# Performance work log

Measured on AMD Instinct MI355X. Metric: run time of the kernel, lower is better.

Reference implementation:

```python
import jax, jax.numpy as jnp
import numpy as np
import math

HEADS = 8
HID = 32
MODES = 8
IN_CH = 4
SEQ = 32
B = 2
H = 64
W = 64


def spectral_conv(x, wr, wi):
    # x: [N, Cin, H, W]; w: [Cin, Cout, m, m] complex (low rfft2 modes only)
    n, _, h, w = x.shape
    m = wr.shape[2]
    xf = jnp.fft.rfft2(x)  # [N, Cin, H, W//2+1] complex64
    of = jnp.einsum('bixy,ioxy->boxy', xf[:, :, :m, :m], wr + 1j * wi)
    out_ft = jnp.zeros((n, wr.shape[1], h, w // 2 + 1), dtype=of.dtype)
    out_ft = out_ft.at[:, :, :m, :m].set(of)
    return jnp.fft.irfft2(out_ft, s=(h, w))


def conv1x1(x, w, b):
    # x: [N, Cin, H, W], w: [Cout, Cin], b: [Cout]
    return jnp.einsum('bchw,oc->bohw', x, w) + b[None, :, None, None]


def setup_inputs() -> dict:
    key = jax.random.key(0)
    ks = jax.random.split(key, 16)
    hd = HEADS * HID
    s = 0.02
    inp = {
        'v': jax.random.normal(ks[0], (B, SEQ, IN_CH, H, W), dtype=jnp.float32),
        'qwr': jax.random.normal(ks[1], (IN_CH, hd, MODES, MODES), dtype=jnp.float32) * s,
        'qwi': jax.random.normal(ks[2], (IN_CH, hd, MODES, MODES), dtype=jnp.float32) * s,
        'kwr': jax.random.normal(ks[3], (IN_CH, hd, MODES, MODES), dtype=jnp.float32) * s,
        'kwi': jax.random.normal(ks[4], (IN_CH, hd, MODES, MODES), dtype=jnp.float32) * s,
        'vwr': jax.random.normal(ks[5], (IN_CH, hd, MODES, MODES), dtype=jnp.float32) * s,
        'vwi': jax.random.normal(ks[6], (IN_CH, hd, MODES, MODES), dtype=jnp.float32) * s,
        'u1wr': jax.random.normal(ks[7], (hd, HID, MODES, MODES), dtype=jnp.float32) * s,
        'u1wi': jax.random.normal(ks[8], (hd, HID, MODES, MODES), dtype=jnp.float32) * s,
        'u2wr': jax.random.normal(ks[9], (HID, IN_CH, MODES, MODES), dtype=jnp.float32) * s,
        'u2wi': jax.random.normal(ks[10], (HID, IN_CH, MODES, MODES), dtype=jnp.float32) * s,
        's1w': jax.random.normal(ks[11], (HID, hd), dtype=jnp.float32) * s,
        's1b': jnp.zeros((HID,), dtype=jnp.float32),
        's2w': jax.random.normal(ks[12], (IN_CH, HID), dtype=jnp.float32) * s,
        's2b': jnp.zeros((IN_CH,), dtype=jnp.float32),
    }
    return inp


def reference(v, qwr, qwi, kwr, kwi, vwr, vwi, u1wr, u1wi, u2wr, u2wi, s1w, s1b, s2w, s2b):
    b, s, c, h, w = v.shape
    scale = 1.0 / math.sqrt(HID / HEADS)
    vr = v.reshape(b * s, c, h, w)
    embed = (b, HEADS, s, -1, h, w)  # same raw row-major reshape as torch
    q = spectral_conv(vr, qwr, qwi).reshape(embed)
    k = spectral_conv(vr, kwr, kwi).reshape(embed)
    val = spectral_conv(vr, vwr, vwi).reshape(embed)
    # inner products over channel dim, then dx^2-weighted spatial integral
    ip = jnp.einsum('bhsdrc,bhtdrc->bhstrc', q, k) * scale
    dx = 1.0 / h
    l2 = jnp.sum(ip, axis=(-2, -1)) * (dx * dx)  # [b, h, s1, s2]
    A = jax.nn.softmax(l2, axis=-1)
    u = jnp.einsum('bhst,bhtdrc->bhsdrc', A, val)
    u = jnp.transpose(u, (0, 2, 1, 3, 4, 5)).reshape(b * s, HEADS * u.shape[3], h, w)
    # SimpleFNO: gelu(conv1) + skip1, then conv2 + skip2
    x1 = jax.nn.gelu(spectral_conv(u, u1wr, u1wi), approximate=False) + conv1x1(u, s1w, s1b)
    x2 = spectral_conv(x1, u2wr, u2wi) + conv1x1(x1, s2w, s2b)
    return x2.reshape(b, s, c, h, w)
```

## Files before the change

### kernel.cpp

```cpp
#include <hip/hip_runtime.h>
#include <math.h>

#define HEADS 8
#define HIDC  32
#define MODES 8
#define IN_CH 4
#define SEQ   32
#define NS    64
#define HD    256
#define NM    64
#define NPIX  4096
#define TWO_PI_D 6.283185307179586476925286766559

__device__ __forceinline__ float2 f2(float a, float b){ return make_float2(a,b); }

__global__ __launch_bounds__(256) void fwd_dft_kernel(const float* __restrict__ src,
                                                      float2* __restrict__ dst){
  int f = blockIdx.x;
  const float* fld = src + (size_t)f * NPIX;
  __shared__ float  s_fld[64*65];
  __shared__ float2 s_cs[64];
  __shared__ float2 s_a1[64][8];
  int tid = threadIdx.x;
  for (int k = tid; k < NPIX; k += 256) s_fld[(k>>6)*65 + (k&63)] = fld[k];
  if (tid < 64){ double sv, cv; sincos(TWO_PI_D * tid / 64.0, &sv, &cv); s_cs[tid] = f2((float)cv,(float)sv); }
  __syncthreads();
  for (int o = tid; o < 512; o += 256){
    int y = o >> 3, kx = o & 7;
    const float* row = s_fld + y*65;
    float sr = 0.f, si = 0.f;
    for (int x = 0; x < 64; ++x){
      float2 cs = s_cs[(kx*x) & 63];
      float v = row[x];
      sr += v * cs.x; si -= v * cs.y;
    }
    s_a1[y][kx] = f2(sr, si);
  }
  __syncthreads();
  if (tid < 64){
    int ky = tid >> 3, kx = tid & 7;
    float sr = 0.f, si = 0.f;
    for (int y = 0; y < 64; ++y){
      float2 a = s_a1[y][kx];
      float2 cs = s_cs[(ky*y) & 63];
      sr += a.x*cs.x + a.y*cs.y;
      si += a.y*cs.x - a.x*cs.y;
    }
    dst[(size_t)f*NM + tid] = f2(sr, si);
  }
}

__global__ __launch_bounds__(256) void gram_kernel(const float* __restrict__ qwr, const float* __restrict__ qwi,
                                                   const float* __restrict__ kwr, const float* __restrict__ kwi,
                                                   float2* __restrict__ G2, float* __restrict__ Gdc){
  int m = blockIdx.x, tid = threadIdx.x;
  __shared__ float qsr[4][257], qsi[4][257], ksr[4][257], ksi[4][257];
  for (int k = tid; k < 1024; k += 256){
    int i = k >> 8, c = k & 255;
    size_t a = ((size_t)(i*256 + c))*64 + m;
    qsr[i][c] = qwr[a]; qsi[i][c] = qwi[a];
    ksr[i][c] = kwr[a]; ksi[i][c] = kwi[a];
  }
  __syncthreads();
  int kx = m & 7, ky = m >> 3;
  float w = (kx >= 1) ? 2.0f : ((ky >= 1) ? 0.5f : 0.0f);
  for (int e = tid; e < 1024; e += 256){
    int P = e >> 7, T = (e >> 4) & 7, i = (e >> 2) & 3, j = e & 3;
    float grr=0.f, gri=0.f, gir=0.f, gii=0.f;
    for (int d = 0; d < 32; ++d){
      float ar = qsr[i][P*32+d], ai = qsi[i][P*32+d];
      float br = ksr[j][T*32+d], bi = ksi[j][T*32+d];
      grr += ar*br; gri += ar*bi; gir += ai*br; gii += ai*bi;
    }
    G2[(size_t)(((m*8+P)*4+i)*4+j)*8 + T] = f2(w*(grr+gii), w*(gir-gri));
    if (m == 0){
      int o = ((P*4+i)*4+j)*8 + T;
      Gdc[o] = grr; Gdc[1024+o] = gri; Gdc[2048+o] = gir; Gdc[3072+o] = gii;
    }
  }
}

__global__ __launch_bounds__(256) void attn_kernel(const float2* __restrict__ Vf,
                                                   const float2* __restrict__ G2,
                                                   const float* __restrict__ Gdc,
                                                   float* __restrict__ A){
  int bx = blockIdx.x;
  int s = bx & 31;
  int base = ((bx >> 8) * 32) + (((bx >> 5) & 7) * 4);
  int tid = threadIdx.x;
  int t = tid & 31, mc = tid >> 5;
  __shared__ float2 s_vf[4][IN_CH][64];
  __shared__ float  s_part[8][33];
  for (int k = tid; k < 4*IN_CH*64; k += 256){
    int m = k & 63, c = (k>>6)&3, smp = k>>8;
    s_vf[smp][c][m] = Vf[((size_t)(base+smp)*IN_CH + c)*NM + m];
  }
  __syncthreads();
  int sg = s >> 3, P = s & 7;
  int tg = t >> 3, T = t & 7;
  float acc = 0.f;
  for (int mm = 0; mm < 8; ++mm){
    int m = mc*8 + mm;
    const float2* g = G2 + (size_t)((m*8+P)*16)*8 + T;
    float sub = 0.f;
    for (int i = 0; i < 4; ++i){
      float2 a = s_vf[sg][i][m];
      for (int j = 0; j < 4; ++j){
        float2 b = s_vf[tg][j][m];
        float zr = a.x*b.x + a.y*b.y;
        float zi = a.y*b.x - a.x*b.y;
        float2 gv = g[(size_t)(i*4+j)*8];
        sub += zr*gv.x - zi*gv.y;
      }
    }
    acc += sub;
  }
  if (mc == 0){
    float sub = 0.f;
    for (int i = 0; i < 4; ++i){
      float2 a = s_vf[sg][i][0];
      for (int j = 0; j < 4; ++j){
        float2 b = s_vf[tg][j][0];
        int o = ((P*4+i)*4+j)*8 + T;
        sub += a.x*b.x*Gdc[o] - a.x*b.y*Gdc[1024+o]
             - a.y*b.x*Gdc[2048+o] + a.y*b.y*Gdc[3072+o];
      }
    }
    acc += sub;
  }
  s_part[mc][t] = acc;
  __syncthreads();
  if (tid < 32){
    float l2 = 0.f;
    for (int k = 0; k < 8; ++k) l2 += s_part[k][tid];
    l2 *= 0.5f / (4096.0f * 4096.0f);
    float mx = l2;
    for (int off = 16; off; off >>= 1) mx = fmaxf(mx, __shfl_xor(mx, off, 32));
    float e = expf(l2 - mx);
    float sm = e;
    for (int off = 16; off; off >>= 1) sm += __shfl_xor(sm, off, 32);
    A[(size_t)bx*32 + tid] = e / sm;
  }
}

__global__ __launch_bounds__(256) void uspec_kernel(const float2* __restrict__ Vf,
                                                    const float* __restrict__ vwr, const float* __restrict__ vwi,
                                                    const float* __restrict__ A,
                                                    float2* __restrict__ Uf){
  int bid = blockIdx.x;
  int mg = bid & 31, hh = (bid >> 5) & 7, b = bid >> 8;
  int m0 = mg*2;
  int nbase = b*32 + hh*4;
  int tid = threadIdx.x;
  __shared__ float2 s_vw[4][2][256];
  __shared__ float2 s_vv[4][2][256];
  __shared__ float  s_A[32][33];
  __shared__ float2 s_vf[4][4][2];
  for (int k = tid; k < 2048; k += 256){
    int i = k >> 9, mm = (k >> 8) & 1, c = k & 255;
    size_t a = ((size_t)i*256 + c)*64 + m0 + mm;
    s_vw[i][mm][c] = f2(vwr[a], vwi[a]);
  }
  for (int k = tid; k < 1024; k += 256)
    s_A[k>>5][k&31] = A[(size_t)((b*8+hh)*32 + (k>>5))*32 + (k&31)];
  if (tid < 32){
    int smp = tid >> 3, i = (tid >> 1) & 3, mm = tid & 1;
    s_vf[smp][i][mm] = Vf[((size_t)(nbase+smp)*4 + i)*64 + m0 + mm];
  }
  __syncthreads();
  for (int k = tid; k < 2048; k += 256){
    int smp = k >> 9, mm = (k >> 8) & 1, c = k & 255;
    float sr = 0.f, si = 0.f;
    for (int i = 0; i < 4; ++i){
      float2 v = s_vf[smp][i][mm];
      float2 w = s_vw[i][mm][c];
      sr += v.x*w.x - v.y*w.y;
      si += v.x*w.y + v.y*w.x;
    }
    s_vv[smp][mm][c] = f2(sr, si);
  }
  __syncthreads();
  int sg = tid >> 5, d = tid & 31;
  float2 acc[4][2];
  for (int ss = 0; ss < 4; ++ss)
    for (int mm = 0; mm < 2; ++mm) acc[ss][mm] = f2(0.f, 0.f);
  for (int tt = 0; tt < 32; ++tt){
    int tg = tt >> 3, c = (tt & 7)*32 + d;
    float a0 = s_A[sg*4+0][tt], a1 = s_A[sg*4+1][tt];
    float a2 = s_A[sg*4+2][tt], a3 = s_A[sg*4+3][tt];
    for (int mm = 0; mm < 2; ++mm){
      float2 v = s_vv[tg][mm][c];
      acc[0][mm].x += a0*v.x; acc[0][mm].y += a0*v.y;
      acc[1][mm].x += a1*v.x; acc[1][mm].y += a1*v.y;
      acc[2][mm].x += a2*v.x; acc[2][mm].y += a2*v.y;
      acc[3][mm].x += a3*v.x; acc[3][mm].y += a3*v.y;
    }
  }
  for (int ss = 0; ss < 4; ++ss){
    int n = b*32 + sg*4 + ss;
    for (int mm = 0; mm < 2; ++mm)
      Uf[((size_t)n*64 + m0 + mm)*256 + hh*32 + d] = acc[ss][mm];
  }
}

__global__ __launch_bounds__(256) void u1t_kernel(const float* __restrict__ u1wr,
                                                  const float* __restrict__ u1wi,
                                                  float4* __restrict__ u1wT){
  int t = blockIdx.x*256 + threadIdx.x;
  int o1 = t & 31, c = (t>>5) & 255, m = t >> 13;
  float pr = ((m & 7)==0 && m) ? 0.5f : 1.0f;
  float pi = m ? pr : 0.0f;
  size_t src = ((size_t)c*32 + o1)*64 + m;
  float wr = u1wr[src], wi = u1wi[src];
  u1wT[t] = make_float4(pr*wr, pi*wi, pr*wi, pi*wr);
}

__global__ __launch_bounds__(128) void mix1_kernel(const float2* __restrict__ Uf,
                                                   const float4* __restrict__ u1wT,
                                                   const float* __restrict__ s1w,
                                                   float2* __restrict__ U1f, float2* __restrict__ S1f){
  int n = blockIdx.x >> 4, mg = blockIdx.x & 15, m0 = mg*4;
  int tid = threadIdx.x;
  __shared__ float2 s_u[4][256];
  for (int k = tid; k < 1024; k += 128){
    int mm = k >> 8, c = k & 255;
    s_u[mm][c] = Uf[((size_t)n*64 + m0 + mm)*256 + c];
  }
  __syncthreads();
  int o1 = tid & 31, mm = tid >> 5;
  int m = m0 + mm;
  const float4* wp = u1wT + (size_t)m*256*32 + o1;
  const float* swp = s1w + o1*256;
  float2 au = f2(0.f,0.f), asv = f2(0.f,0.f);
  #pragma unroll 8
  for (int c = 0; c < 256; ++c){
    float2 u = s_u[mm][c];
    float4 w = wp[(size_t)c*32];
    float sw = swp[c];
    au.x  += u.x*w.x - u.y*w.y;
    au.y  += u.x*w.z + u.y*w.w;
    asv.x += u.x*sw;
    asv.y += u.y*sw;
  }
  size_t ob = ((size_t)n*32 + o1)*64 + m;
  U1f[ob] = au; S1f[ob] = asv;
}

__global__ __launch_bounds__(256) void x1dft_kernel(const float2* __restrict__ U1f,
                                                    const float2* __restrict__ S1f,
                                                    const float* __restrict__ s1b,
                                                    float* __restrict__ x1,
                                                    float2* __restrict__ X1f){
  int f = blockIdx.x, o1 = f & 31, tid = threadIdx.x;
  __shared__ float2 s_e[64][8];
  __shared__ float2 s_gu[64], s_gs[64];
  __shared__ float2 s_tu[64][8], s_ts[64][8];
  __shared__ float  s_fld[64*68];
  __shared__ float2 s_a1[64][8];
  for (int e = tid; e < 512; e += 256){
    int a = e >> 3, b = e & 7;
    double sv, cv; sincos(TWO_PI_D * ((a*b) & 63) / 64.0, &sv, &cv);
    s_e[a][b] = f2((float)cv, (float)sv);
  }
  if (tid >= 128 && tid < 192) s_gu[tid-128] = U1f[(size_t)f*NM + tid-128];
  else if (tid >= 192) s_gs[tid-192] = S1f[(size_t)f*NM + tid-192];
  __syncthreads();
  for (int o = tid; o < 512; o += 256){
    int y = o >> 3, kx = o & 7;
    float wf = (kx ? 2.0f : 1.0f) * (1.0f/4096.0f);
    float ar=0.f, ai=0.f, br=0.f, bi=0.f;
    for (int ky = 0; ky < 8; ++ky){
      float2 cs = s_e[y][ky];
      float2 gu = s_gu[ky*8+kx], gs = s_gs[ky*8+kx];
      ar += gu.x*cs.x - gu.y*cs.y;  ai += gu.x*cs.y + gu.y*cs.x;
      br += gs.x*cs.x - gs.y*cs.y;  bi += gs.x*cs.y + gs.y*cs.x;
    }
    s_tu[y][kx] = f2(ar*wf, ai*wf);
    s_ts[y][kx] = f2(br*wf, bi*wf);
  }
  __syncthreads();
  int xx = tid & 63;
  float2 ce[8];
  {
    const float4* ep = (const float4*)&s_e[xx][0];
    float4 e0 = ep[0], e1 = ep[1], e2 = ep[2], e3 = ep[3];
    ce[0]=f2(e0.x,e0.y); ce[1]=f2(e0.z,e0.w);
    ce[2]=f2(e1.x,e1.y); ce[3]=f2(e1.z,e1.w);
    ce[4]=f2(e2.x,e2.y); ce[5]=f2(e2.z,e2.w);
    ce[6]=f2(e3.x,e3.y); ce[7]=f2(e3.z,e3.w);
  }
  float bias = s1b[o1];
  float* dst = x1 + (size_t)f*NPIX;
  for (int i = 0; i < 16; ++i){
    int p = i*256 + tid;
    int y = p >> 6;
    const float4* tp = (const float4*)&s_tu[y][0];
    float4 t0 = tp[0], t1 = tp[1], t2 = tp[2], t3 = tp[3];
    const float4* up = (const float4*)&s_ts[y][0];
    float4 u0 = up[0], u1 = up[1], u2 = up[2], u3 = up[3];
    float vu = t0.x*ce[0].x - t0.y*ce[0].y + t0.z*ce[1].x - t0.w*ce[1].y
             + t1.x*ce[2].x - t1.y*ce[2].y + t1.z*ce[3].x - t1.w*ce[3].y
             + t2.x*ce[4].x - t2.y*ce[4].y + t2.z*ce[5].x - t2.w*ce[5].y
             + t3.x*ce[6].x - t3.y*ce[6].y + t3.z*ce[7].x - t3.w*ce[7].y;
    float vs = u0.x*ce[0].x - u0.y*ce[0].y + u0.z*ce[1].x - u0.w*ce[1].y
             + u1.x*ce[2].x - u1.y*ce[2].y + u1.z*ce[3].x - u1.w*ce[3].y
             + u2.x*ce[4].x - u2.y*ce[4].y + u2.z*ce[5].x - u2.w*ce[5].y
             + u3.x*ce[6].x - u3.y*ce[6].y + u3.z*ce[7].x - u3.w*ce[7].y;
    float g = 0.5f * vu * (1.0f + erff(vu * 0.70710678f));
    float val = g + vs + bias;
    dst[p] = val;
    s_fld[y*68 + xx] = val;
  }
  __syncthreads();
  for (int o = tid; o < 512; o += 256){
    int y = o >> 3, kx = o & 7;
    const float4* row = (const float4*)&s_fld[y*68];
    float sr = 0.f, si = 0.f;
    for (int x4 = 0; x4 < 16; ++x4){
      float4 v = row[x4];
      int xb = x4*4;
      float2 c0 = s_e[xb+0][kx], c1 = s_e[xb+1][kx];
      float2 c2 = s_e[xb+2][kx], c3 = s_e[xb+3][kx];
      sr += v.x*c0.x + v.y*c1.x + v.z*c2.x + v.w*c3.x;
      si -= v.x*c0.y + v.y*c1.y + v.z*c2.y + v.w*c3.y;
    }
    s_a1[y][kx] = f2(sr, si);
  }
  __syncthreads();
  if (tid < 64){
    int ky = tid >> 3, kx = tid & 7;
    float sr = 0.f, si = 0.f;
    for (int y = 0; y < 64; ++y){
      float2 a = s_a1[y][kx];
      float2 cs = s_e[y][ky];
      sr += a.x*cs.x + a.y*cs.y;
      si += a.y*cs.x - a.x*cs.y;
    }
    X1f[(size_t)f*NM + tid] = f2(sr, si);
  }
}

__global__ __launch_bounds__(256) void final_kernel(const float2* __restrict__ X1f,
                                                    const float* __restrict__ u2wr, const float* __restrict__ u2wi,
                                                    const float* __restrict__ x1,
                                                    const float* __restrict__ s2w, const float* __restrict__ s2b,
                                                    float* __restrict__ out){
  int n = blockIdx.x >> 4, tile = blockIdx.x & 15;
  int tid = threadIdx.x;
  __shared__ float2 s_e[64][8];
  __shared__ float2 s_x2f[4][64];
  __shared__ float2 s_tmp[4][64][8];
  __shared__ float  s_w2[128];
  __shared__ float  s_b2[4];
  for (int e = tid; e < 512; e += 256){
    int a = e >> 3, b = e & 7;
    double sv, cv; sincos(TWO_PI_D * ((a*b) & 63) / 64.0, &sv, &cv);
    s_e[a][b] = f2((float)cv, (float)sv);
  }
  if (tid < 128) s_w2[tid] = s2w[tid];
  if (tid >= 128 && tid < 132) s_b2[tid-128] = s2b[tid-128];
  {
    int o2 = tid >> 6, m = tid & 63;
    float sr = 0.f, si = 0.f;
    for (int o1 = 0; o1 < 32; ++o1){
      float2 xv = X1f[((size_t)n*HIDC + o1)*NM + m];
      size_t wb = ((size_t)(o1*IN_CH + o2))*NM + m;
      float wr = u2wr[wb], wi = u2wi[wb];
      sr += xv.x*wr - xv.y*wi;
      si += xv.x*wi + xv.y*wr;
    }
    s_x2f[o2][m] = f2(sr, si);
  }
  __syncthreads();
  for (int o = tid; o < 2048; o += 256){
    int o2 = o >> 9, rem = o & 511, y = rem >> 3, kx = rem & 7;
    float wf = (kx ? 2.0f : 1.0f) * (1.0f/4096.0f);
    float tr=0.f, ti=0.f;
    for (int ky = 0; ky < 8; ++ky){
      float2 cs = s_e[y][ky];
      float2 g = s_x2f[o2][ky*8+kx];
      tr += g.x*cs.x - g.y*cs.y;
      ti += g.x*cs.y + g.y*cs.x;
    }
    s_tmp[o2][y][kx] = f2(tr*wf, ti*wf);
  }
  __syncthreads();
  int p = tile*256 + tid;
  int y = p >> 6, xx = p & 63;
  float2 ce[8];
  {
    const float4* ep = (const float4*)&s_e[xx][0];
    float4 e0 = ep[0], e1 = ep[1], e2 = ep[2], e3 = ep[3];
    ce[0]=f2(e0.x,e0.y); ce[1]=f2(e0.z,e0.w);
    ce[2]=f2(e1.x,e1.y); ce[3]=f2(e1.z,e1.w);
    ce[4]=f2(e2.x,e2.y); ce[5]=f2(e2.z,e2.w);
    ce[6]=f2(e3.x,e3.y); ce[7]=f2(e3.z,e3.w);
  }
  const float* xbase = x1 + (size_t)n*HIDC*NPIX;
  float* obase = out + (size_t)n*IN_CH*NPIX;
  float a0 = s_b2[0], a1 = s_b2[1], a2 = s_b2[2], a3 = s_b2[3];
  #pragma unroll 8
  for (int c = 0; c < 32; ++c){
    float xv = xbase[(size_t)c*NPIX + p];
    a0 += s_w2[c]*xv; a1 += s_w2[32+c]*xv; a2 += s_w2[64+c]*xv; a3 += s_w2[96+c]*xv;
  }
  float sp[4];
  #pragma unroll
  for (int o2 = 0; o2 < 4; ++o2){
    const float4* tp = (const float4*)&s_tmp[o2][y][0];
    float4 t0 = tp[0], t1 = tp[1], t2 = tp[2], t3 = tp[3];
    sp[o2] = t0.x*ce[0].x - t0.y*ce[0].y + t0.z*ce[1].x - t0.w*ce[1].y
           + t1.x*ce[2].x - t1.y*ce[2].y + t1.z*ce[3].x - t1.w*ce[3].y
           + t2.x*ce[4].x - t2.y*ce[4].y + t2.z*ce[5].x - t2.w*ce[5].y
           + t3.x*ce[6].x - t3.y*ce[6].y + t3.z*ce[7].x - t3.w*ce[7].y;
  }
  obase[p]          = a0 + sp[0];
  obase[NPIX + p]   = a1 + sp[1];
  obase[2*NPIX + p] = a2 + sp[2];
  obase[3*NPIX + p] = a3 + sp[3];
}

extern "C" void kernel_launch(void* const* d_in, const int* in_sizes, int n_in,
                              void* d_out, int out_size, void* d_ws, size_t ws_size,
                              hipStream_t stream) {
  (void)in_sizes; (void)n_in; (void)out_size; (void)ws_size;
  const float* v    = (const float*)d_in[0];
  const float* qwr  = (const float*)d_in[1];
  const float* qwi  = (const float*)d_in[2];
  const float* kwr  = (const float*)d_in[3];
  const float* kwi  = (const float*)d_in[4];
  const float* vwr  = (const float*)d_in[5];
  const float* vwi  = (const float*)d_in[6];
  const float* u1wr = (const float*)d_in[7];
  const float* u1wi = (const float*)d_in[8];
  const float* u2wr = (const float*)d_in[9];
  const float* u2wi = (const float*)d_in[10];
  const float* s1w  = (const float*)d_in[11];
  const float* s1b  = (const float*)d_in[12];
  const float* s2w  = (const float*)d_in[13];
  const float* s2b  = (const float*)d_in[14];
  float* out = (float*)d_out;

  float* ws = (float*)d_ws;
  size_t off = 0;
  float2* Vf   = (float2*)(ws + off); off += (size_t)NS*IN_CH*NM*2;
  float2* G2   = (float2*)(ws + off); off += (size_t)65536*2;
  float*  Gdc  =          (ws + off); off += 4096;
  float*  A    =          (ws + off); off += 16384;
  float2* Uf   = (float2*)(ws + off); off += (size_t)NS*NM*HD*2;
  float2* U1f  = (float2*)(ws + off); off += (size_t)NS*HIDC*NM*2;
  float2* S1f  = (float2*)(ws + off); off += (size_t)NS*HIDC*NM*2;
  float*  x1   =          (ws + off); off += (size_t)NS*HIDC*NPIX;
  float2* X1f  = (float2*)(ws + off); off += (size_t)NS*HIDC*NM*2;
  float4* u1wT = (float4*)x1;

  fwd_dft_kernel<<<NS*IN_CH, 256, 0, stream>>>(v, Vf);
  gram_kernel<<<64, 256, 0, stream>>>(qwr, qwi, kwr, kwi, G2, Gdc);
  u1t_kernel<<<2048, 256, 0, stream>>>(u1wr, u1wi, u1wT);
  attn_kernel<<<512, 256, 0, stream>>>(Vf, G2, Gdc, A);
  uspec_kernel<<<512, 256, 0, stream>>>(Vf, vwr, vwi, A, Uf);
  mix1_kernel<<<1024, 128, 0, stream>>>(Uf, u1wT, s1w, U1f, S1f);
  x1dft_kernel<<<NS*HIDC, 256, 0, stream>>>(U1f, S1f, s1b, x1, X1f);
  final_kernel<<<64*16, 256, 0, stream>>>(X1f, u2wr, u2wi, x1, s2w, s2b, out);
}
```

Baseline: 227.2 us.

## Eliminate x1 materialization by splitting linear skip path into spectral domain

The linear skip branch (conv1x1 of u plus bias) is band-limited, so its contribution to the second spectral conv and to the final 1x1 conv is computed directly from S1f modes, with the bias folded into the DC term. This removes the full-resolution x1 write and re-read. The final kernel now recomputes the GELU branch per 4-row tile from U1f modes and applies the s2w mix to it. A precomputed twiddle table kernel replaces per-block double-precision sincos, and the forward DFT is vectorized with float4 loads. The trade-off is redundant per-tile inverse-DFT and erf work in the final kernel in place of memory traffic.

Measured after the change: 222.0 us. 2.3% less time.

```diff
diff --git a/kernel.cpp b/kernel.cpp
--- a/kernel.cpp
+++ b/kernel.cpp
@@ -14,25 +14,40 @@
 
 __device__ __forceinline__ float2 f2(float a, float b){ return make_float2(a,b); }
 
+__global__ void twiddle_kernel(float2* __restrict__ Etab){
+  int t = threadIdx.x;
+  int a = t >> 3, b = t & 7;
+  double sv, cv; sincos(TWO_PI_D * ((a*b) & 63) / 64.0, &sv, &cv);
+  Etab[t] = f2((float)cv, (float)sv);
+}
+
 __global__ __launch_bounds__(256) void fwd_dft_kernel(const float* __restrict__ src,
+                                                      const float2* __restrict__ Etab,
                                                       float2* __restrict__ dst){
-  int f = blockIdx.x;
-  const float* fld = src + (size_t)f * NPIX;
-  __shared__ float  s_fld[64*65];
-  __shared__ float2 s_cs[64];
+  int f = blockIdx.x, tid = threadIdx.x;
+  __shared__ float  s_fld[64*68];
+  __shared__ float2 s_e[64][8];
   __shared__ float2 s_a1[64][8];
-  int tid = threadIdx.x;
-  for (int k = tid; k < NPIX; k += 256) s_fld[(k>>6)*65 + (k&63)] = fld[k];
-  if (tid < 64){ double sv, cv; sincos(TWO_PI_D * tid / 64.0, &sv, &cv); s_cs[tid] = f2((float)cv,(float)sv); }
+  for (int e = tid; e < 512; e += 256) ((float2*)s_e)[e] = Etab[e];
+  const float4* f4 = (const float4*)(src + (size_t)f*NPIX);
+  for (int k = tid; k < 1024; k += 256){
+    float4 v = f4[k];
+    int y = k >> 4, x4 = (k & 15)*4;
+    float* row = &s_fld[y*68 + x4];
+    row[0]=v.x; row[1]=v.y; row[2]=v.z; row[3]=v.w;
+  }
   __syncthreads();
   for (int o = tid; o < 512; o += 256){
     int y = o >> 3, kx = o & 7;
-    const float* row = s_fld + y*65;
+    const float4* row = (const float4*)&s_fld[y*68];
     float sr = 0.f, si = 0.f;
-    for (int x = 0; x < 64; ++x){
-      float2 cs = s_cs[(kx*x) & 63];
-      float v = row[x];
-      sr += v * cs.x; si -= v * cs.y;
+    for (int x4 = 0; x4 < 16; ++x4){
+      float4 v = row[x4];
+      int xb = x4*4;
+      float2 c0 = s_e[xb+0][kx], c1 = s_e[xb+1][kx];
+      float2 c2 = s_e[xb+2][kx], c3 = s_e[xb+3][kx];
+      sr += v.x*c0.x + v.y*c1.x + v.z*c2.x + v.w*c3.x;
+      si -= v.x*c0.y + v.y*c1.y + v.z*c2.y + v.w*c3.y;
     }
     s_a1[y][kx] = f2(sr, si);
   }
@@ -42,7 +57,7 @@
     float sr = 0.f, si = 0.f;
     for (int y = 0; y < 64; ++y){
       float2 a = s_a1[y][kx];
-      float2 cs = s_cs[(ky*y) & 63];
+      float2 cs = s_e[y][ky];
       sr += a.x*cs.x + a.y*cs.y;
       si += a.y*cs.x - a.x*cs.y;
     }
@@ -246,70 +261,46 @@
   U1f[ob] = au; S1f[ob] = asv;
 }
 
-__global__ __launch_bounds__(256) void x1dft_kernel(const float2* __restrict__ U1f,
-                                                    const float2* __restrict__ S1f,
-                                                    const float* __restrict__ s1b,
-                                                    float* __restrict__ x1,
-                                                    float2* __restrict__ X1f){
-  int f = blockIdx.x, o1 = f & 31, tid = threadIdx.x;
+__global__ __launch_bounds__(256) void xg_kernel(const float2* __restrict__ Etab,
+                                                 const float2* __restrict__ U1f,
+                                                 float2* __restrict__ Xg){
+  int f = blockIdx.x, tid = threadIdx.x;
   __shared__ float2 s_e[64][8];
-  __shared__ float2 s_gu[64], s_gs[64];
-  __shared__ float2 s_tu[64][8], s_ts[64][8];
+  __shared__ float2 s_gu[64];
+  __shared__ float2 s_tu[64][8];
   __shared__ float  s_fld[64*68];
   __shared__ float2 s_a1[64][8];
-  for (int e = tid; e < 512; e += 256){
-    int a = e >> 3, b = e & 7;
-    double sv, cv; sincos(TWO_PI_D * ((a*b) & 63) / 64.0, &sv, &cv);
-    s_e[a][b] = f2((float)cv, (float)sv);
-  }
-  if (tid >= 128 && tid < 192) s_gu[tid-128] = U1f[(size_t)f*NM + tid-128];
-  else if (tid >= 192) s_gs[tid-192] = S1f[(size_t)f*NM + tid-192];
+  for (int e = tid; e < 512; e += 256) ((float2*)s_e)[e] = Etab[e];
+  if (tid < 64) s_gu[tid] = U1f[(size_t)f*NM + tid];
   __syncthreads();
   for (int o = tid; o < 512; o += 256){
     int y = o >> 3, kx = o & 7;
     float wf = (kx ? 2.0f : 1.0f) * (1.0f/4096.0f);
-    float ar=0.f, ai=0.f, br=0.f, bi=0.f;
+    float ar=0.f, ai=0.f;
     for (int ky = 0; ky < 8; ++ky){
       float2 cs = s_e[y][ky];
-      float2 gu = s_gu[ky*8+kx], gs = s_gs[ky*8+kx];
-      ar += gu.x*cs.x - gu.y*cs.y;  ai += gu.x*cs.y + gu.y*cs.x;
-      br += gs.x*cs.x - gs.y*cs.y;  bi += gs.x*cs.y + gs.y*cs.x;
+      float2 gu = s_gu[ky*8+kx];
+      ar += gu.x*cs.x - gu.y*cs.y;
+      ai += gu.x*cs.y + gu.y*cs.x;
     }
     s_tu[y][kx] = f2(ar*wf, ai*wf);
-    s_ts[y][kx] = f2(br*wf, bi*wf);
   }
   __syncthreads();
   int xx = tid & 63;
   float2 ce[8];
-  {
-    const float4* ep = (const float4*)&s_e[xx][0];
-    float4 e0 = ep[0], e1 = ep[1], e2 = ep[2], e3 = ep[3];
-    ce[0]=f2(e0.x,e0.y); ce[1]=f2(e0.z,e0.w);
-    ce[2]=f2(e1.x,e1.y); ce[3]=f2(e1.z,e1.w);
-    ce[4]=f2(e2.x,e2.y); ce[5]=f2(e2.z,e2.w);
-    ce[6]=f2(e3.x,e3.y); ce[7]=f2(e3.z,e3.w);
-  }
-  float bias = s1b[o1];
-  float* dst = x1 + (size_t)f*NPIX;
+  #pragma unroll
+  for (int k = 0; k < 8; ++k) ce[k] = s_e[xx][k];
   for (int i = 0; i < 16; ++i){
     int p = i*256 + tid;
     int y = p >> 6;
     const float4* tp = (const float4*)&s_tu[y][0];
     float4 t0 = tp[0], t1 = tp[1], t2 = tp[2], t3 = tp[3];
-    const float4* up = (const float4*)&s_ts[y][0];
-    float4 u0 = up[0], u1 = up[1], u2 = up[2], u3 = up[3];
     float vu = t0.x*ce[0].x - t0.y*ce[0].y + t0.z*ce[1].x - t0.w*ce[1].y
              + t1.x*ce[2].x - t1.y*ce[2].y + t1.z*ce[3].x - t1.w*ce[3].y
              + t2.x*ce[4].x - t2.y*ce[4].y + t2.z*ce[5].x - t2.w*ce[5].y
              + t3.x*ce[6].x - t3.y*ce[6].y + t3.z*ce[7].x - t3.w*ce[7].y;
-    float vs = u0.x*ce[0].x - u0.y*ce[0].y + u0.z*ce[1].x - u0.w*ce[1].y
-             + u1.x*ce[2].x - u1.y*ce[2].y + u1.z*ce[3].x - u1.w*ce[3].y
-             + u2.x*ce[4].x - u2.y*ce[4].y + u2.z*ce[5].x - u2.w*ce[5].y
-             + u3.x*ce[6].x - u3.y*ce[6].y + u3.z*ce[7].x - u3.w*ce[7].y;
     float g = 0.5f * vu * (1.0f + erff(vu * 0.70710678f));
-    float val = g + vs + bias;
-    dst[p] = val;
-    s_fld[y*68 + xx] = val;
+    s_fld[y*68 + xx] = g;
   }
   __syncthreads();
   for (int o = tid; o < 512; o += 256){
@@ -336,88 +327,114 @@
       sr += a.x*cs.x + a.y*cs.y;
       si += a.y*cs.x - a.x*cs.y;
     }
-    X1f[(size_t)f*NM + tid] = f2(sr, si);
-  }
-}
-
-__global__ __launch_bounds__(256) void final_kernel(const float2* __restrict__ X1f,
+    Xg[(size_t)f*NM + tid] = f2(sr, si);
+  }
+}
+
+__global__ __launch_bounds__(256) void final_kernel(const float2* __restrict__ Etab,
+                                                    const float2* __restrict__ U1f,
+                                                    const float2* __restrict__ S1f,
+                                                    const float2* __restrict__ Xg,
                                                     const float* __restrict__ u2wr, const float* __restrict__ u2wi,
-                                                    const float* __restrict__ x1,
+                                                    const float* __restrict__ s1b,
                                                     const float* __restrict__ s2w, const float* __restrict__ s2b,
                                                     float* __restrict__ out){
-  int n = blockIdx.x >> 4, tile = blockIdx.x & 15;
+  int n = blockIdx.x >> 4, tile = blockIdx.x & 15, y0 = tile*4;
   int tid = threadIdx.x;
   __shared__ float2 s_e[64][8];
-  __shared__ float2 s_x2f[4][64];
-  __shared__ float2 s_tmp[4][64][8];
-  __shared__ float  s_w2[128];
-  __shared__ float  s_b2[4];
-  for (int e = tid; e < 512; e += 256){
-    int a = e >> 3, b = e & 7;
-    double sv, cv; sincos(TWO_PI_D * ((a*b) & 63) / 64.0, &sv, &cv);
-    s_e[a][b] = f2((float)cv, (float)sv);
-  }
+  __shared__ float2 s_u1[32][64];
+  __shared__ float2 s_T[32][4][8];
+  __shared__ float2 s_os[4][64];
+  __shared__ float2 s_tmp[4][4][8];
+  __shared__ float  s_w2[128], s_s1b[32], s_b2[4];
+  for (int e = tid; e < 512; e += 256) ((float2*)s_e)[e] = Etab[e];
+  for (int k = tid; k < 2048; k += 256) ((float2*)s_u1)[k] = U1f[(size_t)n*2048 + k];
   if (tid < 128) s_w2[tid] = s2w[tid];
-  if (tid >= 128 && tid < 132) s_b2[tid-128] = s2b[tid-128];
+  else if (tid < 160) s_s1b[tid-128] = s1b[tid-128];
+  else if (tid < 164) s_b2[tid-160] = s2b[tid-160];
+  __syncthreads();
+  for (int e = tid; e < 1024; e += 256){
+    int c = e >> 5, yy = (e >> 3) & 3, kx = e & 7;
+    int y = y0 + yy;
+    float wf = (kx ? 2.0f : 1.0f) * (1.0f/4096.0f);
+    float ar = 0.f, ai = 0.f;
+    for (int ky = 0; ky < 8; ++ky){
+      float2 cs = s_e[y][ky];
+      float2 g = s_u1[c][ky*8+kx];
+      ar += g.x*cs.x - g.y*cs.y;
+      ai += g.x*cs.y + g.y*cs.x;
+    }
+    s_T[c][yy][kx] = f2(ar*wf, ai*wf);
+  }
   {
     int o2 = tid >> 6, m = tid & 63;
-    float sr = 0.f, si = 0.f;
+    float prm = ((m & 7)==0 && m) ? 0.5f : 1.0f;
+    float pim = m ? prm : 0.0f;
+    float dc = (m == 0) ? 4096.0f : 0.0f;
+    float cr = 0.f, ci = 0.f;
     for (int o1 = 0; o1 < 32; ++o1){
-      float2 xv = X1f[((size_t)n*HIDC + o1)*NM + m];
+      float2 xg = Xg[((size_t)n*32 + o1)*NM + m];
+      float2 sf = S1f[((size_t)n*32 + o1)*NM + m];
+      float Xr = xg.x + sf.x*prm + dc*s_s1b[o1];
+      float Xi = xg.y + sf.y*pim;
       size_t wb = ((size_t)(o1*IN_CH + o2))*NM + m;
       float wr = u2wr[wb], wi = u2wi[wb];
-      sr += xv.x*wr - xv.y*wi;
-      si += xv.x*wi + xv.y*wr;
-    }
-    s_x2f[o2][m] = f2(sr, si);
-  }
-  __syncthreads();
-  for (int o = tid; o < 2048; o += 256){
-    int o2 = o >> 9, rem = o & 511, y = rem >> 3, kx = rem & 7;
+      float sw = s_w2[o2*32 + o1];
+      cr += Xr*wr - Xi*wi + sw*sf.x;
+      ci += Xr*wi + Xi*wr + sw*sf.y;
+    }
+    s_os[o2][m] = f2(cr, ci);
+  }
+  __syncthreads();
+  if (tid < 128){
+    int o2 = tid >> 5, yy = (tid >> 3) & 3, kx = tid & 7;
+    int y = y0 + yy;
     float wf = (kx ? 2.0f : 1.0f) * (1.0f/4096.0f);
     float tr=0.f, ti=0.f;
     for (int ky = 0; ky < 8; ++ky){
       float2 cs = s_e[y][ky];
-      float2 g = s_x2f[o2][ky*8+kx];
+      float2 g = s_os[o2][ky*8+kx];
       tr += g.x*cs.x - g.y*cs.y;
       ti += g.x*cs.y + g.y*cs.x;
     }
-    s_tmp[o2][y][kx] = f2(tr*wf, ti*wf);
-  }
-  __syncthreads();
-  int p = tile*256 + tid;
-  int y = p >> 6, xx = p & 63;
+    s_tmp[o2][yy][kx] = f2(tr*wf, ti*wf);
+  }
+  __syncthreads();
+  int yy = tid >> 6, xx = tid & 63;
   float2 ce[8];
-  {
-    const float4* ep = (const float4*)&s_e[xx][0];
-    float4 e0 = ep[0], e1 = ep[1], e2 = ep[2], e3 = ep[3];
-    ce[0]=f2(e0.x,e0.y); ce[1]=f2(e0.z,e0.w);
-    ce[2]=f2(e1.x,e1.y); ce[3]=f2(e1.z,e1.w);
-    ce[4]=f2(e2.x,e2.y); ce[5]=f2(e2.z,e2.w);
-    ce[6]=f2(e3.x,e3.y); ce[7]=f2(e3.z,e3.w);
-  }
-  const float* xbase = x1 + (size_t)n*HIDC*NPIX;
-  float* obase = out + (size_t)n*IN_CH*NPIX;
+  #pragma unroll
+  for (int k = 0; k < 8; ++k) ce[k] = s_e[xx][k];
   float a0 = s_b2[0], a1 = s_b2[1], a2 = s_b2[2], a3 = s_b2[3];
-  #pragma unroll 8
   for (int c = 0; c < 32; ++c){
-    float xv = xbase[(size_t)c*NPIX + p];
-    a0 += s_w2[c]*xv; a1 += s_w2[32+c]*xv; a2 += s_w2[64+c]*xv; a3 += s_w2[96+c]*xv;
+    float b = s_s1b[c];
+    a0 += s_w2[c]*b; a1 += s_w2[32+c]*b; a2 += s_w2[64+c]*b; a3 += s_w2[96+c]*b;
+  }
+  for (int c = 0; c < 32; ++c){
+    const float4* tp = (const float4*)&s_T[c][yy][0];
+    float4 t0 = tp[0], t1 = tp[1], t2 = tp[2], t3 = tp[3];
+    float vu = t0.x*ce[0].x - t0.y*ce[0].y + t0.z*ce[1].x - t0.w*ce[1].y
+             + t1.x*ce[2].x - t1.y*ce[2].y + t1.z*ce[3].x - t1.w*ce[3].y
+             + t2.x*ce[4].x - t2.y*ce[4].y + t2.z*ce[5].x - t2.w*ce[5].y
+             + t3.x*ce[6].x - t3.y*ce[6].y + t3.z*ce[7].x - t3.w*ce[7].y;
+    float g = 0.5f * vu * (1.0f + erff(vu * 0.70710678f));
+    a0 += s_w2[c]*g; a1 += s_w2[32+c]*g; a2 += s_w2[64+c]*g; a3 += s_w2[96+c]*g;
   }
   float sp[4];
   #pragma unroll
   for (int o2 = 0; o2 < 4; ++o2){
-    const float4* tp = (const float4*)&s_tmp[o2][y][0];
+    const float4* tp = (const float4*)&s_tmp[o2][yy][0];
     float4 t0 = tp[0], t1 = tp[1], t2 = tp[2], t3 = tp[3];
     sp[o2] = t0.x*ce[0].x - t0.y*ce[0].y + t0.z*ce[1].x - t0.w*ce[1].y
            + t1.x*ce[2].x - t1.y*ce[2].y + t1.z*ce[3].x - t1.w*ce[3].y
            + t2.x*ce[4].x - t2.y*ce[4].y + t2.z*ce[5].x - t2.w*ce[5].y
            + t3.x*ce[6].x - t3.y*ce[6].y + t3.z*ce[7].x - t3.w*ce[7].y;
   }
-  obase[p]          = a0 + sp[0];
-  obase[NPIX + p]   = a1 + sp[1];
-  obase[2*NPIX + p] = a2 + sp[2];
-  obase[3*NPIX + p] = a3 + sp[3];
+  int p = (y0 + yy)*64 + xx;
+  float* ob = out + (size_t)n*IN_CH*NPIX;
+  ob[p]          = a0 + sp[0];
+  ob[NPIX + p]   = a1 + sp[1];
+  ob[2*NPIX + p] = a2 + sp[2];
+  ob[3*NPIX + p] = a3 + sp[3];
 }
 
 extern "C" void kernel_launch(void* const* d_in, const int* in_sizes, int n_in,
@@ -443,6 +460,7 @@
 
   float* ws = (float*)d_ws;
   size_t off = 0;
+  float2* Etab =(float2*)(ws + off); off += 1024;
   float2* Vf   = (float2*)(ws + off); off += (size_t)NS*IN_CH*NM*2;
   float2* G2   = (float2*)(ws + off); off += (size_t)65536*2;
   float*  Gdc  =          (ws + off); off += 4096;
@@ -450,16 +468,16 @@
   float2* Uf   = (float2*)(ws + off); off += (size_t)NS*NM*HD*2;
   float2* U1f  = (float2*)(ws + off); off += (size_t)NS*HIDC*NM*2;
   float2* S1f  = (float2*)(ws + off); off += (size_t)NS*HIDC*NM*2;
-  float*  x1   =          (ws + off); off += (size_t)NS*HIDC*NPIX;
-  float2* X1f  = (float2*)(ws + off); off += (size_t)NS*HIDC*NM*2;
-  float4* u1wT = (float4*)x1;
-
-  fwd_dft_kernel<<<NS*IN_CH, 256, 0, stream>>>(v, Vf);
+  float2* Xg   = (float2*)(ws + off); off += (size_t)NS*HIDC*NM*2;
+  float4* u1wT = (float4*)(ws + off); off += (size_t)524288*4;
+
+  twiddle_kernel<<<1, 512, 0, stream>>>(Etab);
+  fwd_dft_kernel<<<NS*IN_CH, 256, 0, stream>>>(v, Etab, Vf);
   gram_kernel<<<64, 256, 0, stream>>>(qwr, qwi, kwr, kwi, G2, Gdc);
   u1t_kernel<<<2048, 256, 0, stream>>>(u1wr, u1wi, u1wT);
   attn_kernel<<<512, 256, 0, stream>>>(Vf, G2, Gdc, A);
   uspec_kernel<<<512, 256, 0, stream>>>(Vf, vwr, vwi, A, Uf);
   mix1_kernel<<<1024, 128, 0, stream>>>(Uf, u1wT, s1w, U1f, S1f);
-  x1dft_kernel<<<NS*HIDC, 256, 0, stream>>>(U1f, S1f, s1b, x1, X1f);
-  final_kernel<<<64*16, 256, 0, stream>>>(X1f, u2wr, u2wi, x1, s2w, s2b, out);
-}
+  xg_kernel<<<NS*HIDC, 256, 0, stream>>>(Etab, U1f, Xg);
+  final_kernel<<<NS*16, 256, 0, stream>>>(Etab, U1f, S1f, Xg, u2wr, u2wi, s1b, s2w, s2b, out);
+}
```
